# Kernel tuning notes

Measured on AMD Instinct MI355X. Metric: run time of the kernel, lower is better.

Reference implementation:

```python
import jax, jax.numpy as jnp
import numpy as np
from jax import lax

STRIDE = (1, 1)
PADDING = ((1, 1), (1, 1))
DILATION = (1, 1)


def setup_inputs() -> dict:
    key = jax.random.key(0)
    k1, k2 = jax.random.split(key)
    input = jax.random.normal(k1, (32, 128, 56, 56), dtype=jnp.float32)
    weight = jax.random.normal(k2, (256, 128, 3, 3), dtype=jnp.float32)
    bias = jnp.zeros((256,), dtype=jnp.float32)
    return {"input": input, "weight": weight, "bias": bias}


def reference(input, weight, bias):
    # The original builds the conv's dense matrix via conv2d on an identity
    # basis and then matmuls; that is mathematically identical to a direct
    # conv2d (the map is linear), plus the broadcast bias.
    out = lax.conv_general_dilated(
        input, weight,
        window_strides=STRIDE,
        padding=PADDING,
        rhs_dilation=DILATION,
        dimension_numbers=("NCHW", "OIHW", "NCHW"),
    )
    return out + bias[None, :, None, None]
```

## Files before the change

### kernel.cpp

```cpp
#include <hip/hip_runtime.h>
#include <hip/hip_bf16.h>
#include <stdint.h>


typedef __attribute__((ext_vector_type(8))) short bf16x8;
typedef __attribute__((ext_vector_type(8))) unsigned short ushort8;
typedef __attribute__((ext_vector_type(4))) float f32x4;

#define HW       56
#define SPATIAL  3136
#define C_IN     128
#define K_OUT    256
#define GEMM_K   1152
#define GEMM_N   100352

#define PHW      58
#define PIMG     3364
#define PADTOT_AL 107656

#define BM       256
#define BN       256
#define NTILE    18
#define BUFH     32768

__device__ __forceinline__ unsigned short f2bf(float f) {
    union { float f; unsigned int u; } v; v.f = f;
    unsigned int u = v.u + 0x7FFFu + ((v.u >> 16) & 1u);
    return (unsigned short)(u >> 16);
}

__device__ __forceinline__ void gload16(const unsigned short* g, unsigned short* l) {
    __builtin_amdgcn_global_load_lds(
        (const __attribute__((address_space(1))) unsigned int*)(g),
        (__attribute__((address_space(3))) unsigned int*)(l),
        16, 0, 0);
}

__global__ void wtrans_kernel(const float* __restrict__ w, unsigned short* __restrict__ w3) {
    int idx = blockIdx.x * 256 + threadIdx.x;
    int rc   = idx / 18432;
    int rem  = idx % 18432;
    int tap  = rem / 2048;
    int rem2 = rem % 2048;
    int cc   = rem2 / 512;
    int s    = rem2 % 512;
    int l    = s >> 3, j = s & 7;
    int ko   = rc * 16 + (l & 15);
    int c    = cc * 32 + ((l >> 4) << 3) + j;
    w3[idx] = f2bf(w[(ko * C_IN + c) * 9 + tap]);
}

__global__ __launch_bounds__(256)
void border_zero(unsigned short* __restrict__ pad) {
    int idx = blockIdx.x * 256 + threadIdx.x;
    if (idx >= 29184) return;
    int cc  = idx / 7296;
    int r   = idx % 7296;
    int img = r / 228;
    int p   = r % 228;
    int pos;
    if (p < 58)       pos = p;
    else if (p < 116) pos = 57 * PHW + (p - 58);
    else { int i = p - 116; pos = (1 + (i >> 1)) * PHW + (i & 1) * 57; }
    unsigned short* d = pad + (size_t)cc * PADTOT_AL * 32
                      + ((size_t)img * PIMG + pos) * 32;
    const ushort8 z = (ushort8){0,0,0,0,0,0,0,0};
    *reinterpret_cast<ushort8*>(d)      = z;
    *reinterpret_cast<ushort8*>(d + 8)  = z;
    *reinterpret_cast<ushort8*>(d + 16) = z;
    *reinterpret_cast<ushort8*>(d + 24) = z;
}

__global__ __launch_bounds__(256)
void intrans_kernel(const float* __restrict__ in, unsigned short* __restrict__ pad) {
    __shared__ __attribute__((aligned(16))) unsigned short l[56 * 136];
    const int bx = blockIdx.x;
    const int n = bx / HW, h = bx % HW;
    const int tid = threadIdx.x;
    const float* src = in + (size_t)n * C_IN * SPATIAL + h * HW;
    #pragma unroll
    for (int i = 0; i < 28; ++i) {
        int idx = i * 256 + tid;
        int c = idx / HW, w = idx % HW;
        l[w * 136 + c] = f2bf(src[(size_t)c * SPATIAL + w]);
    }
    __syncthreads();
    const int prow = n * PIMG + (h + 1) * PHW;
    #pragma unroll
    for (int j = 0; j < 4; ++j) {
        int chunk = j * 256 + tid;
        if (chunk < 896) {
            int w = chunk >> 4, c8 = chunk & 15;
            int cc = c8 >> 2, sub = c8 & 3;
            unsigned short* dst = pad + (size_t)cc * PADTOT_AL * 32
                                + (size_t)(prow + w + 1) * 32 + sub * 8;
            *reinterpret_cast<ushort8*>(dst) =
                *reinterpret_cast<const ushort8*>(&l[w * 136 + c8 * 8]);
        }
    }
}

__global__ __launch_bounds__(512, 2)
void conv_m256(const unsigned short* __restrict__ pad,
               const unsigned short* __restrict__ w3,
               const float* __restrict__ bias,
               float* __restrict__ out) {
    __shared__ __attribute__((aligned(16))) unsigned short lds[2 * BUFH];

    const int tid  = threadIdx.x;
    const int wave = tid >> 6;
    const int lane = tid & 63;
    const int la   = lane & 15;
    const int lkh  = lane >> 4;

    const int bid = blockIdx.x;
    const int nt  = (bid & 7) * 49 + (bid >> 3);
    const int g0  = nt * BN;

    const int wr = wave >> 2, wc = wave & 3;

    const unsigned short* aw0 = w3 + (size_t)(wave * 2 + 0) * 18432 + lane * 8;
    const unsigned short* aw1 = w3 + (size_t)(wave * 2 + 1) * 18432 + lane * 8;
    const unsigned short* bsrc0;
    const unsigned short* bsrc1;
    {
        int col = g0 + (wave * 2 + 0) * 16 + la;
        int img = col / SPATIAL;
        int pos = col - img * SPATIAL;
        int oh  = pos / HW, ow = pos - oh * HW;
        bsrc0 = pad + (size_t)(img * PIMG + (oh + 1) * PHW + (ow + 1)) * 32 + lkh * 8;
        col = g0 + (wave * 2 + 1) * 16 + la;
        img = col / SPATIAL;
        pos = col - img * SPATIAL;
        oh  = pos / HW; ow = pos - oh * HW;
        bsrc1 = pad + (size_t)(img * PIMG + (oh + 1) * PHW + (ow + 1)) * 32 + lkh * 8;
    }

    f32x4 acc[8][4];
    #pragma unroll
    for (int i = 0; i < 8; ++i)
        #pragma unroll
        for (int j = 0; j < 4; ++j)
            acc[i][j] = (f32x4){0.f, 0.f, 0.f, 0.f};

    auto STAGE = [&](int tn, int kc) {
        const int tap = tn >> 1;
        const int cc  = (tn & 1) * 2 + kc;
        const int dr = tap / 3 - 1, dsx = tap % 3 - 1;
        unsigned short* dst = &lds[(tn & 1) * BUFH];
        const ptrdiff_t bofs = (ptrdiff_t)cc * PADTOT_AL * 32 + (dr * PHW + dsx) * 32;
        gload16(aw0 + (size_t)(tap * 4 + cc) * 512, dst + ((wave * 2 + 0) * 2 + kc) * 512);
        gload16(aw1 + (size_t)(tap * 4 + cc) * 512, dst + ((wave * 2 + 1) * 2 + kc) * 512);
        gload16(bsrc0 + bofs, dst + 16384 + ((wave * 2 + 0) * 2 + kc) * 512);
        gload16(bsrc1 + bofs, dst + 16384 + ((wave * 2 + 1) * 2 + kc) * 512);
    };

    bf16x8 af0[8], af1[8], bv0[4], bv1[4];

    STAGE(0, 0); STAGE(0, 1); STAGE(1, 0);
    asm volatile("s_waitcnt vmcnt(4)" ::: "memory");
    __builtin_amdgcn_s_barrier();

    #pragma unroll
    for (int t = 0; t < NTILE; ++t) {
        const unsigned short* Ab = &lds[(t & 1) * BUFH];

        #pragma unroll
        for (int mi = 0; mi < 8; ++mi)
            af0[mi] = *reinterpret_cast<const bf16x8*>(
                &Ab[((wr * 8 + mi) * 2 + 0) * 512 + lane * 8]);
        #pragma unroll
        for (int nj = 0; nj < 4; ++nj)
            bv0[nj] = *reinterpret_cast<const bf16x8*>(
                &Ab[16384 + ((wc * 4 + nj) * 2 + 0) * 512 + lane * 8]);
        #pragma unroll
        for (int mi = 0; mi < 8; ++mi)
            af1[mi] = *reinterpret_cast<const bf16x8*>(
                &Ab[((wr * 8 + mi) * 2 + 1) * 512 + lane * 8]);

        asm volatile("s_waitcnt lgkmcnt(8)" ::: "memory");
        __builtin_amdgcn_sched_barrier(0);
        __builtin_amdgcn_s_setprio(1);
        #pragma unroll
        for (int mi = 0; mi < 8; ++mi)
            #pragma unroll
            for (int nj = 0; nj < 4; ++nj)
                acc[mi][nj] = __builtin_amdgcn_mfma_f32_16x16x32_bf16(
                    af0[mi], bv0[nj], acc[mi][nj], 0, 0, 0);
        __builtin_amdgcn_s_setprio(0);

        __builtin_amdgcn_s_barrier();

        #pragma unroll
        for (int nj = 0; nj < 4; ++nj)
            bv1[nj] = *reinterpret_cast<const bf16x8*>(
                &Ab[16384 + ((wc * 4 + nj) * 2 + 1) * 512 + lane * 8]);
        if (t + 1 < NTILE) STAGE(t + 1, 1);
        if (t + 2 < NTILE) STAGE(t + 2, 0);

        asm volatile("s_waitcnt lgkmcnt(0)" ::: "memory");
        __builtin_amdgcn_sched_barrier(0);
        __builtin_amdgcn_s_setprio(1);
        #pragma unroll
        for (int mi = 0; mi < 8; ++mi)
            #pragma unroll
            for (int nj = 0; nj < 4; ++nj)
                acc[mi][nj] = __builtin_amdgcn_mfma_f32_16x16x32_bf16(
                    af1[mi], bv1[nj], acc[mi][nj], 0, 0, 0);
        __builtin_amdgcn_s_setprio(0);

        if (t < NTILE - 2) {
            asm volatile("s_waitcnt vmcnt(4)" ::: "memory");
            __builtin_amdgcn_s_barrier();
        } else if (t == NTILE - 2) {
            asm volatile("s_waitcnt vmcnt(0)" ::: "memory");
            __builtin_amdgcn_s_barrier();
        }
    }

    #pragma unroll
    for (int mi = 0; mi < 8; ++mi) {
        const int mb = wr * 128 + mi * 16 + lkh * 4;
        const f32x4 bv4 = *reinterpret_cast<const f32x4*>(&bias[mb]);
        #pragma unroll
        for (int nj = 0; nj < 4; ++nj) {
            const int gcol = g0 + wc * 64 + nj * 16;
            const int n2 = gcol / SPATIAL;
            const int p2 = gcol - n2 * SPATIAL + la;
            float* op = out + ((size_t)(n2 * K_OUT + mb)) * SPATIAL + p2;
            op[0]                   = acc[mi][nj][0] + bv4[0];
            op[SPATIAL]             = acc[mi][nj][1] + bv4[1];
            op[2 * SPATIAL]         = acc[mi][nj][2] + bv4[2];
            op[3 * (size_t)SPATIAL] = acc[mi][nj][3] + bv4[3];
        }
    }
}

#define LDK 40
__global__ __launch_bounds__(256)
void conv_mfma_fallback(const float* __restrict__ in,
                        const float* __restrict__ wraw,
                        const float* __restrict__ bias,
                        float* __restrict__ out) {
    __shared__ __attribute__((aligned(16))) unsigned short lA[128 * LDK];
    __shared__ __attribute__((aligned(16))) unsigned short lB[128 * LDK];
    const int tid = threadIdx.x;
    const int m0  = blockIdx.y * 128;
    const int g0  = blockIdx.x * 128;
    const int wave = tid >> 6, lane = tid & 63;
    const int wr = wave >> 1, wc = wave & 1;
    const int la = lane & 15, lkh = lane >> 4, lk = lkh * 8;

    f32x4 acc[4][4];
    #pragma unroll
    for (int i = 0; i < 4; ++i)
        #pragma unroll
        for (int j = 0; j < 4; ++j)
            acc[i][j] = (f32x4){0.f, 0.f, 0.f, 0.f};

    const int jj = tid & 127;
    const int kb = (tid >> 7) * 16;
    const int g = g0 + jj;
    const int nimg = g / SPATIAL;
    const int pos  = g % SPATIAL;
    const int oh = pos / HW, ow = pos % HW;

    for (int tap = 0; tap < 9; ++tap) {
        const int dr = tap / 3 - 1, dsx = tap % 3 - 1;
        const int ih = oh + dr, iw = ow + dsx;
        const bool valid = ((unsigned)ih < HW) && ((unsigned)iw < HW);
        const float* src = in + ((nimg * C_IN) * HW + ih) * HW + iw;
        for (int c0 = 0; c0 < C_IN; c0 += 32) {
            #pragma unroll
            for (int i = 0; i < 2; ++i) {
                const int ch = tid * 2 + i;
                const int row = ch >> 2;
                const int kp = (ch & 3) * 8;
                ushort8 v;
                #pragma unroll
                for (int e = 0; e < 8; ++e)
                    v[e] = f2bf(wraw[((m0 + row) * C_IN + c0 + kp + e) * 9 + tap]);
                *reinterpret_cast<ushort8*>(&lA[row * LDK + kp]) = v;
            }
            {
                ushort8 v0, v1;
                #pragma unroll
                for (int i = 0; i < 8; ++i)
                    v0[i] = f2bf(valid ? src[(c0 + kb + i) * SPATIAL] : 0.f);
                #pragma unroll
                for (int i = 0; i < 8; ++i)
                    v1[i] = f2bf(valid ? src[(c0 + kb + 8 + i) * SPATIAL] : 0.f);
                *reinterpret_cast<ushort8*>(&lB[jj * LDK + kb])     = v0;
                *reinterpret_cast<ushort8*>(&lB[jj * LDK + kb + 8]) = v1;
            }
            __syncthreads();
            bf16x8 af[4], bv[4];
            #pragma unroll
            for (int f = 0; f < 4; ++f) {
                af[f] = *reinterpret_cast<const bf16x8*>(&lA[(wr * 64 + f * 16 + la) * LDK + lk]);
                bv[f] = *reinterpret_cast<const bf16x8*>(&lB[(wc * 64 + f * 16 + la) * LDK + lk]);
            }
            #pragma unroll
            for (int fi = 0; fi < 4; ++fi)
                #pragma unroll
                for (int fj = 0; fj < 4; ++fj)
                    acc[fi][fj] = __builtin_amdgcn_mfma_f32_16x16x32_bf16(
                        af[fi], bv[fj], acc[fi][fj], 0, 0, 0);
            __syncthreads();
        }
    }
    const int mbase = m0 + wr * 64;
    const int cbase = g0 + wc * 64;
    #pragma unroll
    for (int fi = 0; fi < 4; ++fi) {
        float bvv[4];
        #pragma unroll
        for (int r = 0; r < 4; ++r)
            bvv[r] = bias[mbase + fi * 16 + lkh * 4 + r];
        #pragma unroll
        for (int fj = 0; fj < 4; ++fj) {
            const int gcol = cbase + fj * 16 + la;
            const int n2 = gcol / SPATIAL;
            const int p2 = gcol % SPATIAL;
            float* op = out + (size_t)(n2 * K_OUT) * SPATIAL + p2;
            #pragma unroll
            for (int r = 0; r < 4; ++r)
                op[(size_t)(mbase + fi * 16 + lkh * 4 + r) * SPATIAL] = acc[fi][fj][r] + bvv[r];
        }
    }
}

extern "C" void kernel_launch(void* const* d_in, const int* in_sizes, int n_in,
                              void* d_out, int out_size, void* d_ws, size_t ws_size,
                              hipStream_t stream) {
    const float* in   = (const float*)d_in[0];
    const float* w    = (const float*)d_in[1];
    const float* bias = (const float*)d_in[2];
    float* out = (float*)d_out;

    const size_t pad_halves = 4ull * PADTOT_AL * 32ull;
    const size_t need_bytes = (pad_halves + 294912ull) * 2ull;

    if (ws_size >= need_bytes) {
        unsigned short* pad = (unsigned short*)d_ws;
        unsigned short* w3  = pad + pad_halves;
        border_zero<<<114, 256, 0, stream>>>(pad);
        wtrans_kernel<<<294912 / 256, 256, 0, stream>>>(w, w3);
        intrans_kernel<<<32 * HW, 256, 0, stream>>>(in, pad);
        conv_m256<<<GEMM_N / BN, 512, 0, stream>>>(pad, w3, bias, out);
    } else {
        dim3 grid(GEMM_N / 128, K_OUT / 128);
        conv_mfma_fallback<<<grid, 256, 0, stream>>>(in, w, bias, out);
    }
}
```

Before: 98.21 us.

## Shrink conv GEMM tile to 128x128 with 256 threads and fuse prep kernels

Reworks the implicit-GEMM convolution from 256x256 tiles with 8 waves to 128x128 tiles with 4 waves. The grid becomes 1568 blocks split across two M halves, with a swizzled block index and halved LDS buffers. This raises block count and occupancy but lowers per-block data reuse and doubles the global traffic for input tiles. It also merges the weight-transform and border-zero kernels into a single launch to save one kernel launch.

```diff
diff --git a/kernel.cpp b/kernel.cpp
--- a/kernel.cpp
+++ b/kernel.cpp
@@ -18,10 +18,8 @@
 #define PIMG     3364
 #define PADTOT_AL 107656
 
-#define BM       256
-#define BN       256
 #define NTILE    18
-#define BUFH     32768
+#define BUFH     16384
 
 __device__ __forceinline__ unsigned short f2bf(float f) {
     union { float f; unsigned int u; } v; v.f = f;
@@ -36,39 +34,40 @@
         16, 0, 0);
 }
 
-__global__ void wtrans_kernel(const float* __restrict__ w, unsigned short* __restrict__ w3) {
-    int idx = blockIdx.x * 256 + threadIdx.x;
-    int rc   = idx / 18432;
-    int rem  = idx % 18432;
-    int tap  = rem / 2048;
-    int rem2 = rem % 2048;
-    int cc   = rem2 / 512;
-    int s    = rem2 % 512;
-    int l    = s >> 3, j = s & 7;
-    int ko   = rc * 16 + (l & 15);
-    int c    = cc * 32 + ((l >> 4) << 3) + j;
-    w3[idx] = f2bf(w[(ko * C_IN + c) * 9 + tap]);
-}
-
 __global__ __launch_bounds__(256)
-void border_zero(unsigned short* __restrict__ pad) {
-    int idx = blockIdx.x * 256 + threadIdx.x;
-    if (idx >= 29184) return;
-    int cc  = idx / 7296;
-    int r   = idx % 7296;
-    int img = r / 228;
-    int p   = r % 228;
-    int pos;
-    if (p < 58)       pos = p;
-    else if (p < 116) pos = 57 * PHW + (p - 58);
-    else { int i = p - 116; pos = (1 + (i >> 1)) * PHW + (i & 1) * 57; }
-    unsigned short* d = pad + (size_t)cc * PADTOT_AL * 32
-                      + ((size_t)img * PIMG + pos) * 32;
-    const ushort8 z = (ushort8){0,0,0,0,0,0,0,0};
-    *reinterpret_cast<ushort8*>(d)      = z;
-    *reinterpret_cast<ushort8*>(d + 8)  = z;
-    *reinterpret_cast<ushort8*>(d + 16) = z;
-    *reinterpret_cast<ushort8*>(d + 24) = z;
+void prep_kernel(const float* __restrict__ w, unsigned short* __restrict__ w3,
+                 unsigned short* __restrict__ pad) {
+    if (blockIdx.x < 1152) {
+        int idx = blockIdx.x * 256 + threadIdx.x;
+        int rc   = idx / 18432;
+        int rem  = idx % 18432;
+        int tap  = rem / 2048;
+        int rem2 = rem % 2048;
+        int cc   = rem2 / 512;
+        int s    = rem2 % 512;
+        int l    = s >> 3, j = s & 7;
+        int ko   = rc * 16 + (l & 15);
+        int c    = cc * 32 + ((l >> 4) << 3) + j;
+        w3[idx] = f2bf(w[(ko * C_IN + c) * 9 + tap]);
+    } else {
+        int idx = (blockIdx.x - 1152) * 256 + threadIdx.x;
+        if (idx >= 29184) return;
+        int cc  = idx / 7296;
+        int r   = idx % 7296;
+        int img = r / 228;
+        int p   = r % 228;
+        int pos;
+        if (p < 58)       pos = p;
+        else if (p < 116) pos = 57 * PHW + (p - 58);
+        else { int i = p - 116; pos = (1 + (i >> 1)) * PHW + (i & 1) * 57; }
+        unsigned short* d = pad + (size_t)cc * PADTOT_AL * 32
+                          + ((size_t)img * PIMG + pos) * 32;
+        const ushort8 z = (ushort8){0,0,0,0,0,0,0,0};
+        *reinterpret_cast<ushort8*>(d)      = z;
+        *reinterpret_cast<ushort8*>(d + 8)  = z;
+        *reinterpret_cast<ushort8*>(d + 16) = z;
+        *reinterpret_cast<ushort8*>(d + 24) = z;
+    }
 }
 
 __global__ __launch_bounds__(256)
@@ -100,11 +99,11 @@
     }
 }
 
-__global__ __launch_bounds__(512, 2)
-void conv_m256(const unsigned short* __restrict__ pad,
-               const unsigned short* __restrict__ w3,
-               const float* __restrict__ bias,
-               float* __restrict__ out) {
+__global__ __launch_bounds__(256, 2)
+void conv_kd(const unsigned short* __restrict__ pad,
+             const unsigned short* __restrict__ w3,
+             const float* __restrict__ bias,
+             float* __restrict__ out) {
     __shared__ __attribute__((aligned(16))) unsigned short lds[2 * BUFH];
 
     const int tid  = threadIdx.x;
@@ -114,13 +113,15 @@
     const int lkh  = lane >> 4;
 
     const int bid = blockIdx.x;
-    const int nt  = (bid & 7) * 49 + (bid >> 3);
-    const int g0  = nt * BN;
-
-    const int wr = wave >> 2, wc = wave & 3;
-
-    const unsigned short* aw0 = w3 + (size_t)(wave * 2 + 0) * 18432 + lane * 8;
-    const unsigned short* aw1 = w3 + (size_t)(wave * 2 + 1) * 18432 + lane * 8;
+    const int swz = (bid & 7) * 196 + (bid >> 3);
+    const int mt  = swz & 1, nt = swz >> 1;
+    const int m0  = mt * 128;
+    const int g0  = nt * 128;
+
+    const int wr = wave >> 1, wc = wave & 1;
+
+    const unsigned short* aw0 = w3 + (size_t)(mt * 8 + wave * 2 + 0) * 18432 + lane * 8;
+    const unsigned short* aw1 = w3 + (size_t)(mt * 8 + wave * 2 + 1) * 18432 + lane * 8;
     const unsigned short* bsrc0;
     const unsigned short* bsrc1;
     {
@@ -136,9 +137,9 @@
         bsrc1 = pad + (size_t)(img * PIMG + (oh + 1) * PHW + (ow + 1)) * 32 + lkh * 8;
     }
 
-    f32x4 acc[8][4];
-    #pragma unroll
-    for (int i = 0; i < 8; ++i)
+    f32x4 acc[4][4];
+    #pragma unroll
+    for (int i = 0; i < 4; ++i)
         #pragma unroll
         for (int j = 0; j < 4; ++j)
             acc[i][j] = (f32x4){0.f, 0.f, 0.f, 0.f};
@@ -148,14 +149,14 @@
         const int cc  = (tn & 1) * 2 + kc;
         const int dr = tap / 3 - 1, dsx = tap % 3 - 1;
         unsigned short* dst = &lds[(tn & 1) * BUFH];
-        const ptrdiff_t bofs = (ptrdiff_t)cc * PADTOT_AL * 32 + (dr * PHW + dsx) * 32;
+        const ptrdiff_t bofs = (ptrdiff_t)cc * (PADTOT_AL * 32) + (dr * PHW + dsx) * 32;
         gload16(aw0 + (size_t)(tap * 4 + cc) * 512, dst + ((wave * 2 + 0) * 2 + kc) * 512);
         gload16(aw1 + (size_t)(tap * 4 + cc) * 512, dst + ((wave * 2 + 1) * 2 + kc) * 512);
-        gload16(bsrc0 + bofs, dst + 16384 + ((wave * 2 + 0) * 2 + kc) * 512);
-        gload16(bsrc1 + bofs, dst + 16384 + ((wave * 2 + 1) * 2 + kc) * 512);
+        gload16(bsrc0 + bofs, dst + 8192 + ((wave * 2 + 0) * 2 + kc) * 512);
+        gload16(bsrc1 + bofs, dst + 8192 + ((wave * 2 + 1) * 2 + kc) * 512);
     };
 
-    bf16x8 af0[8], af1[8], bv0[4], bv1[4];
+    bf16x8 af0[4], af1[4], bv0[4], bv1[4];
 
     STAGE(0, 0); STAGE(0, 1); STAGE(1, 0);
     asm volatile("s_waitcnt vmcnt(4)" ::: "memory");
@@ -166,23 +167,23 @@
         const unsigned short* Ab = &lds[(t & 1) * BUFH];
 
         #pragma unroll
-        for (int mi = 0; mi < 8; ++mi)
+        for (int mi = 0; mi < 4; ++mi)
             af0[mi] = *reinterpret_cast<const bf16x8*>(
-                &Ab[((wr * 8 + mi) * 2 + 0) * 512 + lane * 8]);
+                &Ab[((wr * 4 + mi) * 2 + 0) * 512 + lane * 8]);
         #pragma unroll
         for (int nj = 0; nj < 4; ++nj)
             bv0[nj] = *reinterpret_cast<const bf16x8*>(
-                &Ab[16384 + ((wc * 4 + nj) * 2 + 0) * 512 + lane * 8]);
-        #pragma unroll
-        for (int mi = 0; mi < 8; ++mi)
+                &Ab[8192 + ((wc * 4 + nj) * 2 + 0) * 512 + lane * 8]);
+        #pragma unroll
+        for (int mi = 0; mi < 4; ++mi)
             af1[mi] = *reinterpret_cast<const bf16x8*>(
-                &Ab[((wr * 8 + mi) * 2 + 1) * 512 + lane * 8]);
-
-        asm volatile("s_waitcnt lgkmcnt(8)" ::: "memory");
+                &Ab[((wr * 4 + mi) * 2 + 1) * 512 + lane * 8]);
+
+        asm volatile("s_waitcnt lgkmcnt(4)" ::: "memory");
         __builtin_amdgcn_sched_barrier(0);
         __builtin_amdgcn_s_setprio(1);
         #pragma unroll
-        for (int mi = 0; mi < 8; ++mi)
+        for (int mi = 0; mi < 4; ++mi)
             #pragma unroll
             for (int nj = 0; nj < 4; ++nj)
                 acc[mi][nj] = __builtin_amdgcn_mfma_f32_16x16x32_bf16(
@@ -194,7 +195,7 @@
         #pragma unroll
         for (int nj = 0; nj < 4; ++nj)
             bv1[nj] = *reinterpret_cast<const bf16x8*>(
-                &Ab[16384 + ((wc * 4 + nj) * 2 + 1) * 512 + lane * 8]);
+                &Ab[8192 + ((wc * 4 + nj) * 2 + 1) * 512 + lane * 8]);
         if (t + 1 < NTILE) STAGE(t + 1, 1);
         if (t + 2 < NTILE) STAGE(t + 2, 0);
 
@@ -202,7 +203,7 @@
         __builtin_amdgcn_sched_barrier(0);
         __builtin_amdgcn_s_setprio(1);
         #pragma unroll
-        for (int mi = 0; mi < 8; ++mi)
+        for (int mi = 0; mi < 4; ++mi)
             #pragma unroll
             for (int nj = 0; nj < 4; ++nj)
                 acc[mi][nj] = __builtin_amdgcn_mfma_f32_16x16x32_bf16(
@@ -219,8 +220,8 @@
     }
 
     #pragma unroll
-    for (int mi = 0; mi < 8; ++mi) {
-        const int mb = wr * 128 + mi * 16 + lkh * 4;
+    for (int mi = 0; mi < 4; ++mi) {
+        const int mb = m0 + wr * 64 + mi * 16 + lkh * 4;
         const f32x4 bv4 = *reinterpret_cast<const f32x4*>(&bias[mb]);
         #pragma unroll
         for (int nj = 0; nj < 4; ++nj) {
@@ -344,10 +345,9 @@
     if (ws_size >= need_bytes) {
         unsigned short* pad = (unsigned short*)d_ws;
         unsigned short* w3  = pad + pad_halves;
-        border_zero<<<114, 256, 0, stream>>>(pad);
-        wtrans_kernel<<<294912 / 256, 256, 0, stream>>>(w, w3);
+        prep_kernel<<<1152 + 114, 256, 0, stream>>>(w, w3, pad);
         intrans_kernel<<<32 * HW, 256, 0, stream>>>(in, pad);
-        conv_m256<<<GEMM_N / BN, 512, 0, stream>>>(pad, w3, bias, out);
+        conv_kd<<<(GEMM_N / 128) * (K_OUT / 128), 256, 0, stream>>>(pad, w3, bias, out);
     } else {
         dim3 grid(GEMM_N / 128, K_OUT / 128);
         conv_mfma_fallback<<<grid, 256, 0, stream>>>(in, w, bias, out);
```

New measurement: 99.47 us. About the same (+1.3%).
